# Kernel tuning notes

Measured on AMD Instinct MI355X. Metric: run time of the kernel, lower is better.

The kernel has to match this reference:

```python
import jax, jax.numpy as jnp
from jax import lax
import numpy as np

I_CNN = 2048   # box feature dim
Q_H = 1024     # LSTM hidden
Q_E = 300      # word embedding dim
HID = 512      # gated MLP hidden
B = 256
MAXN = 100
T = 14


def setup_inputs() -> dict:
    key = jax.random.key(0)
    ks = jax.random.split(key, 12)
    w = lambda k, shape: (jax.random.normal(k, shape, dtype=jnp.float32) * 0.02)
    return {
        "wholefeat": jax.random.normal(ks[0], (B, I_CNN), dtype=jnp.float32),
        "pooled": jax.random.normal(ks[1], (B, I_CNN), dtype=jnp.float32),
        "box_feats": jax.random.normal(ks[2], (B, MAXN, I_CNN), dtype=jnp.float32),
        "q_feats": jax.random.normal(ks[3], (B, T, Q_E), dtype=jnp.float32),
        "box_coords": jax.random.uniform(ks[4], (B, MAXN, 4), dtype=jnp.float32),
        "index": jax.random.randint(ks[5], (B,), 1, MAXN + 1),
        # LSTM params (PyTorch layout: gates ordered i,f,g,o)
        "W_ih": w(ks[6], (4 * Q_H, Q_E)),
        "W_hh": w(ks[7], (4 * Q_H, Q_H)),
        "b_ih": jnp.zeros((4 * Q_H,), jnp.float32),
        "b_hh": jnp.zeros((4 * Q_H,), jnp.float32),
        # gated MLP params
        "W_w": w(ks[8], (HID, I_CNN + Q_H)),
        "W_b": jnp.zeros((HID,), jnp.float32),
        "Wp_w": w(ks[9], (HID, I_CNN + Q_H)),
        "Wp_b": jnp.zeros((HID,), jnp.float32),
        "f_w": w(ks[10], (1, HID)),
    }


def _lstm_last(x_tbe, W_ih, W_hh, b_ih, b_hh):
    # x_tbe: [T, B, E] time-major. Returns final hidden state h_T: [B, H].
    H = W_hh.shape[1]
    # precompute input projections for all timesteps: [T, B, 4H]
    xg = jnp.einsum('tbe,ge->tbg', x_tbe, W_ih) + (b_ih + b_hh)

    def step(carry, xt):
        h, c = carry
        gates = xt + h @ W_hh.T                       # [B, 4H]
        i, f, g, o = jnp.split(gates, 4, axis=-1)
        i = jax.nn.sigmoid(i)
        f = jax.nn.sigmoid(f)
        g = jnp.tanh(g)
        o = jax.nn.sigmoid(o)
        c = f * c + i * g
        h = o * jnp.tanh(c)
        return (h, c), None

    h0 = jnp.zeros((x_tbe.shape[1], H), x_tbe.dtype)
    (h, _), _ = lax.scan(step, (h0, h0), xg)
    return h


def reference(wholefeat, pooled, box_feats, q_feats, box_coords, index,
              W_ih, W_hh, b_ih, b_hh, W_w, W_b, Wp_w, Wp_b, f_w):
    # question encoding: last LSTM output per sample -> [B, Q_H]
    q_rnn = _lstm_last(jnp.transpose(q_feats, (1, 0, 2)), W_ih, W_hh, b_ih, b_hh)

    Bn, N, _ = box_feats.shape
    qst = jnp.broadcast_to(q_rnn[:, None, :], (Bn, N, q_rnn.shape[-1]))
    b_full = jnp.concatenate([box_feats, qst], axis=-1)        # [B, N, 3072]

    y_tilde = jnp.tanh(jnp.einsum('bnd,hd->bnh', b_full, W_w) + W_b)
    g = jax.nn.sigmoid(jnp.einsum('bnd,hd->bnh', b_full, Wp_w) + Wp_b)
    si = y_tilde * g                                           # [B, N, HID]
    wsi = jax.nn.sigmoid(jnp.einsum('bnh,oh->bno', si, f_w))[..., 0]  # [B, N]

    # ragged reduction: only the first index[i] boxes of sample i contribute
    mask = (jnp.arange(N)[None, :] < index[:, None]).astype(wsi.dtype)
    return jnp.sum(wsi * mask, axis=1)                         # [B]
```

## Files before the change

### kernel.cpp

```cpp
#include <hip/hip_runtime.h>
#include <cstdint>
#include <cstddef>

#define DEVI __device__ __forceinline__

typedef __attribute__((ext_vector_type(8))) short short8;
typedef __attribute__((ext_vector_type(4))) float f32x4;
typedef __bf16 bf16x8 __attribute__((ext_vector_type(8)));

DEVI float sigf(float x) { return 1.0f / (1.0f + __expf(-x)); }
DEVI float tanh_f(float x) { return 2.0f / (1.0f + __expf(-2.0f * x)) - 1.0f; }

DEVI short f2bf(float x) {
    uint32_t u = __builtin_bit_cast(uint32_t, x);
    u += 0x7FFFu + ((u >> 16) & 1u);
    return (short)(u >> 16);
}
DEVI float bf2f(short s) {
    uint32_t u = ((uint32_t)(unsigned short)s) << 16;
    return __builtin_bit_cast(float, u);
}

DEVI void gload16(const void* g, void* l) {
    __builtin_amdgcn_global_load_lds(
        (const __attribute__((address_space(1))) void*)g,
        (__attribute__((address_space(3))) void*)l, 16, 0, 0);
}

DEVI f32x4 mfma16(short8 a, short8 b, f32x4 c) {
    return __builtin_amdgcn_mfma_f32_16x16x32_bf16(
        __builtin_bit_cast(bf16x8, a), __builtin_bit_cast(bf16x8, b), c, 0, 0, 0);
}


__global__ __launch_bounds__(256) void prep_wstk(const float* __restrict__ Wih,
                                                 const float* __restrict__ Whh,
                                                 const float* __restrict__ bih,
                                                 const float* __restrict__ bhh,
                                                 short* __restrict__ Wstk) {
    int idx = blockIdx.x * 256 + threadIdx.x;
    if (idx >= 4096 * 1344) return;
    int n = idx / 1344, k = idx - n * 1344;
    int hblk = n >> 6, gate = (n >> 4) & 3, hl = n & 15;
    int on = gate * 1024 + hblk * 16 + hl;
    float v = 0.f;
    if (k < 300) v = Wih[on * 300 + k];
    else if (k == 300) v = bih[on] + bhh[on];
    else if (k >= 320) v = Whh[on * 1024 + (k - 320)];
    Wstk[idx] = f2bf(v);
}

__global__ __launch_bounds__(256) void prep_x(const float* __restrict__ q,
                                              short* __restrict__ xb) {
    int idx = blockIdx.x * 256 + threadIdx.x;
    if (idx >= 14 * 256 * 320) return;
    int t = idx / (256 * 320);
    int r = idx - t * 256 * 320;
    int b = r / 320, e = r - b * 320;
    float v = (e < 300) ? q[(b * 14 + t) * 300 + e] : (e == 300 ? 1.0f : 0.0f);
    xb[idx] = f2bf(v);
}

__global__ __launch_bounds__(256) void prep_wcat(const float* __restrict__ Ww,
                                                 const float* __restrict__ Wpw,
                                                 short* __restrict__ Wcat) {
    int idx = blockIdx.x * 256 + threadIdx.x;
    if (idx >= 1024 * 3072) return;
    int n = idx / 3072, k = idx - n * 3072;
    int hg = n >> 5, which = (n >> 4) & 1, hl = n & 15;
    int h = hg * 16 + hl;
    const float* src = which ? Wpw : Ww;
    Wcat[idx] = f2bf(src[h * 3072 + k]);
}

__global__ __launch_bounds__(256) void prep_index(const int* __restrict__ index,
                                                  int* __restrict__ cum,
                                                  int* __restrict__ rowmap,
                                                  int* __restrict__ bmap) {
    __shared__ int s[256];
    int t = threadIdx.x;
    int myidx = index[t];
    s[t] = myidx;
    __syncthreads();
    for (int off = 1; off < 256; off <<= 1) {
        int v = (t >= off) ? s[t - off] : 0;
        __syncthreads();
        s[t] += v;
        __syncthreads();
    }
    cum[t + 1] = s[t];
    if (t == 0) cum[0] = 0;
    int base = s[t] - myidx;
    for (int j = 0; j < myidx; ++j) {
        rowmap[base + j] = t * 100 + j;
        bmap[base + j] = t;
    }
    int Ml = s[255];
    if (t < 128) { rowmap[Ml + t] = 0; bmap[Ml + t] = 0; }
}

__global__ __launch_bounds__(256) void compact_box(const float* __restrict__ box,
                                                   const int* __restrict__ index,
                                                   const int* __restrict__ cum,
                                                   short* __restrict__ Ac) {
    int m = blockIdx.x;
    int b = m / 100, j = m - b * 100;
    if (j >= index[b]) return;
    size_t dr = (size_t)(cum[b] + j);
    int t = threadIdx.x;
    const float* src = box + (size_t)m * 2048 + t * 8;
    float4 v0 = *(const float4*)src;
    float4 v1 = *(const float4*)(src + 4);
    short8 s;
    s[0] = f2bf(v0.x); s[1] = f2bf(v0.y); s[2] = f2bf(v0.z); s[3] = f2bf(v0.w);
    s[4] = f2bf(v1.x); s[5] = f2bf(v1.y); s[6] = f2bf(v1.z); s[7] = f2bf(v1.w);
    *(short8*)&Ac[dr * 2048 + t * 8] = s;
}


__global__ __launch_bounds__(256) void xg_gemm(const short* __restrict__ xb,
                                               const short* __restrict__ Wstk,
                                               short* __restrict__ xg) {
    __shared__ __attribute__((aligned(16))) short As[128 * 64];
    __shared__ __attribute__((aligned(16))) short Bs[128 * 64];
    const int tid = threadIdx.x, l = tid & 63, w = tid >> 6;
    const int n0 = blockIdx.x * 128;
    const int m0 = blockIdx.y * 128;
    const int wm = w >> 1, wn = w & 1;

    const short* asrc[4];
    const short* bsrc[4];
    for (int i = 0; i < 4; i++) {
        int r = w * 32 + i * 8 + (l >> 3);
        int cs = (l & 7) ^ (r & 7);
        asrc[i] = xb + (size_t)(m0 + r) * 320 + cs * 8;
        bsrc[i] = Wstk + (size_t)(n0 + r) * 1344 + cs * 8;
    }

    f32x4 acc[4][4];
    for (int i = 0; i < 4; i++)
        for (int j = 0; j < 4; j++) acc[i][j] = f32x4{0.f, 0.f, 0.f, 0.f};

    for (int kt = 0; kt < 5; ++kt) {
        const int k0 = kt * 64;
        __syncthreads();
        for (int i = 0; i < 4; i++)
            gload16(asrc[i] + k0, &As[(w * 32 + i * 8) * 64]);
        for (int i = 0; i < 4; i++)
            gload16(bsrc[i] + k0, &Bs[(w * 32 + i * 8) * 64]);
        __syncthreads();
        for (int ks = 0; ks < 2; ++ks) {
            short8 a[4], b[4];
            for (int mf = 0; mf < 4; ++mf) {
                int m = wm * 64 + mf * 16 + (l & 15);
                int ca = (ks * 4 + (l >> 4)) ^ (m & 7);
                a[mf] = *(const short8*)&As[m * 64 + ca * 8];
            }
            for (int nf = 0; nf < 4; ++nf) {
                int n = wn * 64 + nf * 16 + (l & 15);
                int cb = (ks * 4 + (l >> 4)) ^ (n & 7);
                b[nf] = *(const short8*)&Bs[n * 64 + cb * 8];
            }
            for (int mf = 0; mf < 4; ++mf)
                for (int nf = 0; nf < 4; ++nf)
                    acc[mf][nf] = mfma16(a[mf], b[nf], acc[mf][nf]);
        }
    }
    const int hl = l & 15, hi = l >> 4;
    for (int mf = 0; mf < 4; ++mf)
        for (int nf = 0; nf < 4; ++nf)
            for (int rg = 0; rg < 4; ++rg) {
                int row = m0 + wm * 64 + mf * 16 + hi * 4 + rg;
                int col = n0 + wn * 64 + nf * 16 + hl;
                xg[(size_t)row * 4096 + col] = f2bf(acc[mf][nf][rg]);
            }
}


__global__ __launch_bounds__(128) void lstm_step(const short* __restrict__ hin,
                                                 const short* __restrict__ Wstk,
                                                 const short* __restrict__ xg_t,
                                                 float* __restrict__ c,
                                                 short* __restrict__ hout,
                                                 int dogemm) {
    __shared__ __attribute__((aligned(16))) short As[2][32 * 128];
    __shared__ __attribute__((aligned(16))) short Bs[2][64 * 128];
    const int tid = threadIdx.x, l = tid & 63, w = tid >> 6;
    const int hi = l >> 4, hl = l & 15;
    const int bid = blockIdx.x;
    const int xcd = bid & 7, ii = bid >> 3;
    const int ny = xcd * 8 + (ii & 7);
    const int mx = ii >> 3;
    const int m0 = mx * 32, n0g = ny * 64;

    f32x4 acc[4];
    for (int i = 0; i < 4; i++) acc[i] = f32x4{0.f, 0.f, 0.f, 0.f};

    if (dogemm) {
        const short* asrc[4];
        const short* bsrc[8];
        for (int i = 0; i < 4; i++) {
            int s = i * 128 + tid;
            int r = s >> 4, cs = s & 15;
            asrc[i] = hin + (size_t)(m0 + r) * 1024 + ((cs ^ (r & 15)) * 8);
        }
        for (int i = 0; i < 8; i++) {
            int s = i * 128 + tid;
            int r = s >> 4, cs = s & 15;
            bsrc[i] = Wstk + (size_t)(n0g + r) * 1344 + 320 + ((cs ^ (r & 15)) * 8);
        }
        for (int i = 0; i < 4; i++) gload16(asrc[i], &As[0][(i * 128 + tid) * 8]);
        for (int i = 0; i < 8; i++) gload16(bsrc[i], &Bs[0][(i * 128 + tid) * 8]);

        for (int kt = 0; kt < 8; ++kt) {
            const int cur = kt & 1;
            if (kt < 7) {
                const int k0 = (kt + 1) * 128;
                for (int i = 0; i < 4; i++)
                    gload16(asrc[i] + k0, &As[cur ^ 1][(i * 128 + tid) * 8]);
                for (int i = 0; i < 8; i++)
                    gload16(bsrc[i] + k0, &Bs[cur ^ 1][(i * 128 + tid) * 8]);
                asm volatile("s_waitcnt vmcnt(12)" ::: "memory");
            } else {
                asm volatile("s_waitcnt vmcnt(0)" ::: "memory");
            }
            __builtin_amdgcn_sched_barrier(0);
            __builtin_amdgcn_s_barrier();
            __builtin_amdgcn_sched_barrier(0);
#pragma unroll
            for (int ks = 0; ks < 4; ++ks) {
                const int mrow = w * 16 + hl;
                const int ca = (ks * 4 + hi) ^ hl;
                short8 a = *(const short8*)&As[cur][mrow * 128 + ca * 8];
#pragma unroll
                for (int nf = 0; nf < 4; ++nf) {
                    const int nrow = nf * 16 + hl;
                    short8 b = *(const short8*)&Bs[cur][nrow * 128 + ca * 8];
                    acc[nf] = mfma16(a, b, acc[nf]);
                }
            }
            __builtin_amdgcn_sched_barrier(0);
            asm volatile("s_waitcnt lgkmcnt(0)" ::: "memory");
            __builtin_amdgcn_s_barrier();
            __builtin_amdgcn_sched_barrier(0);
        }
    }

    const short* xr0 = xg_t + (size_t)(m0 + w * 16 + hi * 4) * 4096 + n0g + hl;
    for (int rg = 0; rg < 4; ++rg) {
        const short* xr = xr0 + (size_t)rg * 4096;
        float ig = acc[0][rg] + bf2f(xr[0]);
        float fg = acc[1][rg] + bf2f(xr[16]);
        float gg = acc[2][rg] + bf2f(xr[32]);
        float og = acc[3][rg] + bf2f(xr[48]);
        size_t off = (size_t)(m0 + w * 16 + hi * 4 + rg) * 1024 + ny * 16 + hl;
        float cn = sigf(fg) * c[off] + sigf(ig) * tanh_f(gg);
        c[off] = cn;
        hout[off] = f2bf(sigf(og) * tanh_f(cn));
    }
}


__global__ __launch_bounds__(256) void mlp_gemm(const short* __restrict__ Ac,
                                                const short* __restrict__ hb,
                                                const short* __restrict__ Wcat,
                                                const int* __restrict__ mliveptr,
                                                const int* __restrict__ bmap,
                                                const float* __restrict__ Wb,
                                                const float* __restrict__ Wpb,
                                                const float* __restrict__ fw,
                                                float* __restrict__ logits) {
    __shared__ __attribute__((aligned(16))) short As[128 * 64];
    __shared__ __attribute__((aligned(16))) short Bs[128 * 64];
    const int Mlive = *mliveptr;
    const int tid = threadIdx.x, l = tid & 63, w = tid >> 6;
    const int bid = blockIdx.x;
    const int xcd = bid & 7, ii = bid >> 3;
    const int x = ii & 7, q = ii >> 3;
    const int y = q * 8 + xcd;
    const int n0 = x * 128, m0 = y * 128;
    if (m0 >= Mlive) return;
    const int wm = w >> 1, wn = w & 1;

    const short* asrc[4];
    const short* hsrc[4];
    const short* bsrc[4];
    for (int i = 0; i < 4; i++) {
        int r = w * 32 + i * 8 + (l >> 3);
        int cs = (l & 7) ^ (r & 7);
        asrc[i] = Ac + (size_t)(m0 + r) * 2048 + cs * 8;
        hsrc[i] = hb + (size_t)bmap[m0 + r] * 1024 + cs * 8;
        bsrc[i] = Wcat + (size_t)(n0 + r) * 3072 + cs * 8;
    }

    f32x4 acc[4][4];
    for (int i = 0; i < 4; i++)
        for (int j = 0; j < 4; j++) acc[i][j] = f32x4{0.f, 0.f, 0.f, 0.f};

    for (int kt = 0; kt < 48; ++kt) {
        const int k0 = kt * 64;
        __syncthreads();
        if (kt < 32) {
            for (int i = 0; i < 4; i++)
                gload16(asrc[i] + k0, &As[(w * 32 + i * 8) * 64]);
        } else {
            const int kq = k0 - 2048;
            for (int i = 0; i < 4; i++)
                gload16(hsrc[i] + kq, &As[(w * 32 + i * 8) * 64]);
        }
        for (int i = 0; i < 4; i++)
            gload16(bsrc[i] + k0, &Bs[(w * 32 + i * 8) * 64]);
        __syncthreads();
        for (int ks = 0; ks < 2; ++ks) {
            short8 a[4], b[4];
            for (int mf = 0; mf < 4; ++mf) {
                int m = wm * 64 + mf * 16 + (l & 15);
                int ca = (ks * 4 + (l >> 4)) ^ (m & 7);
                a[mf] = *(const short8*)&As[m * 64 + ca * 8];
            }
            for (int nf = 0; nf < 4; ++nf) {
                int n = wn * 64 + nf * 16 + (l & 15);
                int cb = (ks * 4 + (l >> 4)) ^ (n & 7);
                b[nf] = *(const short8*)&Bs[n * 64 + cb * 8];
            }
            for (int mf = 0; mf < 4; ++mf)
                for (int nf = 0; nf < 4; ++nf)
                    acc[mf][nf] = mfma16(a[mf], b[nf], acc[mf][nf]);
        }
    }

    const int hl = l & 15, hi = l >> 4;
    for (int mf = 0; mf < 4; ++mf) {
        float part[4] = {0.f, 0.f, 0.f, 0.f};
        for (int p = 0; p < 2; ++p) {
            int ntg = (n0 + wn * 64) / 16 + 2 * p;
            int hg = ntg >> 1;
            int h = hg * 16 + hl;
            float fwv = fw[h], wbv = Wb[h], wpbv = Wpb[h];
            for (int rg = 0; rg < 4; ++rg) {
                float y2 = tanh_f(acc[mf][2 * p][rg] + wbv);
                float g2 = sigf(acc[mf][2 * p + 1][rg] + wpbv);
                part[rg] += y2 * g2 * fwv;
            }
        }
        for (int rg = 0; rg < 4; ++rg) {
            float v = part[rg];
            v += __shfl_xor(v, 1, 64);
            v += __shfl_xor(v, 2, 64);
            v += __shfl_xor(v, 4, 64);
            v += __shfl_xor(v, 8, 64);
            if (hl == 0) {
                int row = m0 + wm * 64 + mf * 16 + hi * 4 + rg;
                atomicAdd(&logits[row], v);
            }
        }
    }
}

__global__ __launch_bounds__(128) void reduce_out(const float* __restrict__ logits,
                                                  const int* __restrict__ index,
                                                  const int* __restrict__ cum,
                                                  float* __restrict__ out) {
    int b = blockIdx.x, t = threadIdx.x;
    int idx = index[b];
    int base = cum[b];
    float v = 0.f;
    if (t < 100 && t < idx) v = sigf(logits[base + t]);
    for (int m = 32; m; m >>= 1) v += __shfl_down(v, m, 64);
    __shared__ float s[2];
    if ((t & 63) == 0) s[t >> 6] = v;
    __syncthreads();
    if (t == 0) out[b] = s[0] + s[1];
}


extern "C" void kernel_launch(void* const* d_in, const int* in_sizes, int n_in,
                              void* d_out, int out_size, void* d_ws, size_t ws_size,
                              hipStream_t stream) {
    (void)in_sizes; (void)n_in; (void)out_size; (void)ws_size;
    const float* box = (const float*)d_in[2];
    const float* qf  = (const float*)d_in[3];
    const int* index = (const int*)d_in[5];
    const float* Wih = (const float*)d_in[6];
    const float* Whh = (const float*)d_in[7];
    const float* bih = (const float*)d_in[8];
    const float* bhh = (const float*)d_in[9];
    const float* Ww  = (const float*)d_in[10];
    const float* Wb  = (const float*)d_in[11];
    const float* Wpw = (const float*)d_in[12];
    const float* Wpb = (const float*)d_in[13];
    const float* fw  = (const float*)d_in[14];

    char* p = (char*)d_ws;
    short* Wstk = (short*)p;  p += (size_t)4096 * 1344 * 2;
    short* Wcat = (short*)p;  p += (size_t)1024 * 3072 * 2;
    short* xb   = (short*)p;  p += (size_t)3584 * 320 * 2;
    short* hb0  = (short*)p;  p += (size_t)256 * 1024 * 2;
    short* hb1  = (short*)p;  p += (size_t)256 * 1024 * 2;
    short* xg   = (short*)p;  p += (size_t)3584 * 4096 * 2;
    float* c    = (float*)p;  p += (size_t)256 * 1024 * 4;
    int*   cum  = (int*)p;    p += 260 * 4;
    int*   rowmap = (int*)p;  p += (size_t)(25600 + 128) * 4;
    int*   bmap = (int*)p;    p += (size_t)(25600 + 128) * 4;
    float* lgt  = (float*)p;  p += (size_t)25600 * 4;
    p = (char*)(((uintptr_t)p + 255) & ~(uintptr_t)255);
    short* Ac   = (short*)p;  p += (size_t)25600 * 2048 * 2;

    hipMemsetAsync(hb0, 0, (size_t)256 * 1024 * 2, stream);
    hipMemsetAsync(c, 0, (size_t)256 * 1024 * 4, stream);
    hipMemsetAsync(lgt, 0, (size_t)25600 * 4, stream);

    prep_index<<<1, 256, 0, stream>>>(index, cum, rowmap, bmap);
    prep_wstk<<<(4096 * 1344) / 256, 256, 0, stream>>>(Wih, Whh, bih, bhh, Wstk);
    prep_x<<<(14 * 256 * 320) / 256, 256, 0, stream>>>(qf, xb);
    prep_wcat<<<(1024 * 3072) / 256, 256, 0, stream>>>(Ww, Wpw, Wcat);

    compact_box<<<25600, 256, 0, stream>>>(box, index, cum, Ac);

    xg_gemm<<<dim3(32, 28), 256, 0, stream>>>(xb, Wstk, xg);

    short* hbuf[2] = {hb0, hb1};
    for (int t = 0; t < 14; ++t) {
        lstm_step<<<512, 128, 0, stream>>>(
            hbuf[t & 1], Wstk, xg + (size_t)t * 256 * 4096, c,
            hbuf[(t & 1) ^ 1], t == 0 ? 0 : 1);
    }

    mlp_gemm<<<1600, 256, 0, stream>>>(Ac, hb0, Wcat, cum + 256, bmap,
                                       Wb, Wpb, fw, lgt);
    reduce_out<<<256, 128, 0, stream>>>(lgt, index, cum, (float*)d_out);
}
```

Measured before the change: 351.7 us.

## Fuse prep kernels and memsets, double-buffer MLP GEMM LDS loads

Merges the three weight/input conversion kernels and three memsets into a single vectorized prep_all kernel, which cuts launch count and uses 8-wide stores. It also drops the unused rowmap output from prep_index. mlp_gemm now double-buffers its shared-memory tiles, issuing the next k-tile's global_load_lds before computing the current one and waiting with explicit vmcnt, so loads overlap MFMA work. LDS use doubles to 64KB per block, which may lower occupancy.

New measurement: 341.1 us. -3.0%, faster.

```diff
diff --git a/kernel.cpp b/kernel.cpp
--- a/kernel.cpp
+++ b/kernel.cpp
@@ -33,49 +33,85 @@
 }
 
 
-__global__ __launch_bounds__(256) void prep_wstk(const float* __restrict__ Wih,
-                                                 const float* __restrict__ Whh,
-                                                 const float* __restrict__ bih,
-                                                 const float* __restrict__ bhh,
-                                                 short* __restrict__ Wstk) {
-    int idx = blockIdx.x * 256 + threadIdx.x;
-    if (idx >= 4096 * 1344) return;
-    int n = idx / 1344, k = idx - n * 1344;
-    int hblk = n >> 6, gate = (n >> 4) & 3, hl = n & 15;
-    int on = gate * 1024 + hblk * 16 + hl;
-    float v = 0.f;
-    if (k < 300) v = Wih[on * 300 + k];
-    else if (k == 300) v = bih[on] + bhh[on];
-    else if (k >= 320) v = Whh[on * 1024 + (k - 320)];
-    Wstk[idx] = f2bf(v);
-}
-
-__global__ __launch_bounds__(256) void prep_x(const float* __restrict__ q,
-                                              short* __restrict__ xb) {
-    int idx = blockIdx.x * 256 + threadIdx.x;
-    if (idx >= 14 * 256 * 320) return;
-    int t = idx / (256 * 320);
-    int r = idx - t * 256 * 320;
-    int b = r / 320, e = r - b * 320;
-    float v = (e < 300) ? q[(b * 14 + t) * 300 + e] : (e == 300 ? 1.0f : 0.0f);
-    xb[idx] = f2bf(v);
-}
-
-__global__ __launch_bounds__(256) void prep_wcat(const float* __restrict__ Ww,
-                                                 const float* __restrict__ Wpw,
-                                                 short* __restrict__ Wcat) {
-    int idx = blockIdx.x * 256 + threadIdx.x;
-    if (idx >= 1024 * 3072) return;
-    int n = idx / 3072, k = idx - n * 3072;
-    int hg = n >> 5, which = (n >> 4) & 1, hl = n & 15;
-    int h = hg * 16 + hl;
-    const float* src = which ? Wpw : Ww;
-    Wcat[idx] = f2bf(src[h * 3072 + k]);
+#define W_SLOTS   688128
+#define WC_SLOTS  393216
+#define XB_SLOTS  143360
+#define HB_SLOTS  32768
+#define C_SLOTS   65536
+#define LG_SLOTS  6400
+#define PREP_TOT  (W_SLOTS + WC_SLOTS + XB_SLOTS + HB_SLOTS + C_SLOTS + LG_SLOTS)
+
+__global__ __launch_bounds__(256) void prep_all(const float* __restrict__ Wih,
+                                                const float* __restrict__ Whh,
+                                                const float* __restrict__ bih,
+                                                const float* __restrict__ bhh,
+                                                const float* __restrict__ Ww,
+                                                const float* __restrict__ Wpw,
+                                                const float* __restrict__ q,
+                                                short* __restrict__ Wstk,
+                                                short* __restrict__ Wcat,
+                                                short* __restrict__ xb,
+                                                short* __restrict__ hb0,
+                                                float* __restrict__ c,
+                                                float* __restrict__ lgt) {
+    int s = blockIdx.x * 256 + threadIdx.x;
+    if (s < W_SLOTS) {
+        int n = s / 168, c8 = s - n * 168, kb = c8 * 8;
+        int hblk = n >> 6, gate = (n >> 4) & 3, hl = n & 15;
+        int on = gate * 1024 + hblk * 16 + hl;
+        short8 o;
+#pragma unroll
+        for (int e = 0; e < 8; ++e) {
+            int k = kb + e;
+            float v;
+            if (k < 300) v = Wih[on * 300 + k];
+            else if (k == 300) v = bih[on] + bhh[on];
+            else if (k < 320) v = 0.f;
+            else v = Whh[on * 1024 + (k - 320)];
+            o[e] = f2bf(v);
+        }
+        *(short8*)&Wstk[n * 1344 + kb] = o;
+        return;
+    }
+    s -= W_SLOTS;
+    if (s < WC_SLOTS) {
+        int n = s / 384, c8 = s - n * 384, kb = c8 * 8;
+        int hg = n >> 5, which = (n >> 4) & 1, hl = n & 15;
+        int h = hg * 16 + hl;
+        const float* src = (which ? Wpw : Ww) + (size_t)h * 3072 + kb;
+        float4 v0 = *(const float4*)src;
+        float4 v1 = *(const float4*)(src + 4);
+        short8 o;
+        o[0] = f2bf(v0.x); o[1] = f2bf(v0.y); o[2] = f2bf(v0.z); o[3] = f2bf(v0.w);
+        o[4] = f2bf(v1.x); o[5] = f2bf(v1.y); o[6] = f2bf(v1.z); o[7] = f2bf(v1.w);
+        *(short8*)&Wcat[(size_t)n * 3072 + kb] = o;
+        return;
+    }
+    s -= WC_SLOTS;
+    if (s < XB_SLOTS) {
+        int row = s / 40, c8 = s - row * 40, eb = c8 * 8;
+        int t = row / 256, b = row - t * 256;
+        const float* qr = q + (size_t)(b * 14 + t) * 300;
+        short8 o;
+#pragma unroll
+        for (int e = 0; e < 8; ++e) {
+            int ee = eb + e;
+            float v = (ee < 300) ? qr[ee] : (ee == 300 ? 1.0f : 0.0f);
+            o[e] = f2bf(v);
+        }
+        *(short8*)&xb[(size_t)row * 320 + eb] = o;
+        return;
+    }
+    s -= XB_SLOTS;
+    if (s < HB_SLOTS) { ((short8*)hb0)[s] = short8{0,0,0,0,0,0,0,0}; return; }
+    s -= HB_SLOTS;
+    if (s < C_SLOTS) { ((f32x4*)c)[s] = f32x4{0.f,0.f,0.f,0.f}; return; }
+    s -= C_SLOTS;
+    if (s < LG_SLOTS) { ((f32x4*)lgt)[s] = f32x4{0.f,0.f,0.f,0.f}; return; }
 }
 
 __global__ __launch_bounds__(256) void prep_index(const int* __restrict__ index,
                                                   int* __restrict__ cum,
-                                                  int* __restrict__ rowmap,
                                                   int* __restrict__ bmap) {
     __shared__ int s[256];
     int t = threadIdx.x;
@@ -91,12 +127,9 @@
     cum[t + 1] = s[t];
     if (t == 0) cum[0] = 0;
     int base = s[t] - myidx;
-    for (int j = 0; j < myidx; ++j) {
-        rowmap[base + j] = t * 100 + j;
-        bmap[base + j] = t;
-    }
+    for (int j = 0; j < myidx; ++j) bmap[base + j] = t;
     int Ml = s[255];
-    if (t < 128) { rowmap[Ml + t] = 0; bmap[Ml + t] = 0; }
+    if (t < 128) bmap[Ml + t] = 0;
 }
 
 __global__ __launch_bounds__(256) void compact_box(const float* __restrict__ box,
@@ -270,8 +303,8 @@
                                                 const float* __restrict__ Wpb,
                                                 const float* __restrict__ fw,
                                                 float* __restrict__ logits) {
-    __shared__ __attribute__((aligned(16))) short As[128 * 64];
-    __shared__ __attribute__((aligned(16))) short Bs[128 * 64];
+    __shared__ __attribute__((aligned(16))) short As[2][128 * 64];
+    __shared__ __attribute__((aligned(16))) short Bs[2][128 * 64];
     const int Mlive = *mliveptr;
     const int tid = threadIdx.x, l = tid & 63, w = tid >> 6;
     const int bid = blockIdx.x;
@@ -285,48 +318,64 @@
     const short* asrc[4];
     const short* hsrc[4];
     const short* bsrc[4];
+    int ldso[4];
     for (int i = 0; i < 4; i++) {
         int r = w * 32 + i * 8 + (l >> 3);
         int cs = (l & 7) ^ (r & 7);
         asrc[i] = Ac + (size_t)(m0 + r) * 2048 + cs * 8;
         hsrc[i] = hb + (size_t)bmap[m0 + r] * 1024 + cs * 8;
         bsrc[i] = Wcat + (size_t)(n0 + r) * 3072 + cs * 8;
+        ldso[i] = (w * 32 + i * 8) * 64;
     }
 
     f32x4 acc[4][4];
     for (int i = 0; i < 4; i++)
         for (int j = 0; j < 4; j++) acc[i][j] = f32x4{0.f, 0.f, 0.f, 0.f};
 
+    for (int i = 0; i < 4; i++) gload16(asrc[i], &As[0][ldso[i]]);
+    for (int i = 0; i < 4; i++) gload16(bsrc[i], &Bs[0][ldso[i]]);
+
     for (int kt = 0; kt < 48; ++kt) {
-        const int k0 = kt * 64;
-        __syncthreads();
-        if (kt < 32) {
+        const int cur = kt & 1;
+        if (kt < 47) {
+            const int k1 = (kt + 1) * 64;
+            if (kt + 1 < 32) {
+                for (int i = 0; i < 4; i++)
+                    gload16(asrc[i] + k1, &As[cur ^ 1][ldso[i]]);
+            } else {
+                const int kq = k1 - 2048;
+                for (int i = 0; i < 4; i++)
+                    gload16(hsrc[i] + kq, &As[cur ^ 1][ldso[i]]);
+            }
             for (int i = 0; i < 4; i++)
-                gload16(asrc[i] + k0, &As[(w * 32 + i * 8) * 64]);
+                gload16(bsrc[i] + k1, &Bs[cur ^ 1][ldso[i]]);
+            asm volatile("s_waitcnt vmcnt(8)" ::: "memory");
         } else {
-            const int kq = k0 - 2048;
-            for (int i = 0; i < 4; i++)
-                gload16(hsrc[i] + kq, &As[(w * 32 + i * 8) * 64]);
-        }
-        for (int i = 0; i < 4; i++)
-            gload16(bsrc[i] + k0, &Bs[(w * 32 + i * 8) * 64]);
-        __syncthreads();
+            asm volatile("s_waitcnt vmcnt(0)" ::: "memory");
+        }
+        __builtin_amdgcn_sched_barrier(0);
+        __builtin_amdgcn_s_barrier();
+        __builtin_amdgcn_sched_barrier(0);
         for (int ks = 0; ks < 2; ++ks) {
             short8 a[4], b[4];
             for (int mf = 0; mf < 4; ++mf) {
                 int m = wm * 64 + mf * 16 + (l & 15);
                 int ca = (ks * 4 + (l >> 4)) ^ (m & 7);
-                a[mf] = *(const short8*)&As[m * 64 + ca * 8];
+                a[mf] = *(const short8*)&As[cur][m * 64 + ca * 8];
             }
             for (int nf = 0; nf < 4; ++nf) {
                 int n = wn * 64 + nf * 16 + (l & 15);
                 int cb = (ks * 4 + (l >> 4)) ^ (n & 7);
-                b[nf] = *(const short8*)&Bs[n * 64 + cb * 8];
+                b[nf] = *(const short8*)&Bs[cur][n * 64 + cb * 8];
             }
             for (int mf = 0; mf < 4; ++mf)
                 for (int nf = 0; nf < 4; ++nf)
                     acc[mf][nf] = mfma16(a[mf], b[nf], acc[mf][nf]);
         }
+        __builtin_amdgcn_sched_barrier(0);
+        asm volatile("s_waitcnt lgkmcnt(0)" ::: "memory");
+        __builtin_amdgcn_s_barrier();
+        __builtin_amdgcn_sched_barrier(0);
     }
 
     const int hl = l & 15, hi = l >> 4;
@@ -400,20 +449,14 @@
     short* xg   = (short*)p;  p += (size_t)3584 * 4096 * 2;
     float* c    = (float*)p;  p += (size_t)256 * 1024 * 4;
     int*   cum  = (int*)p;    p += 260 * 4;
-    int*   rowmap = (int*)p;  p += (size_t)(25600 + 128) * 4;
     int*   bmap = (int*)p;    p += (size_t)(25600 + 128) * 4;
     float* lgt  = (float*)p;  p += (size_t)25600 * 4;
     p = (char*)(((uintptr_t)p + 255) & ~(uintptr_t)255);
     short* Ac   = (short*)p;  p += (size_t)25600 * 2048 * 2;
 
-    hipMemsetAsync(hb0, 0, (size_t)256 * 1024 * 2, stream);
-    hipMemsetAsync(c, 0, (size_t)256 * 1024 * 4, stream);
-    hipMemsetAsync(lgt, 0, (size_t)25600 * 4, stream);
-
-    prep_index<<<1, 256, 0, stream>>>(index, cum, rowmap, bmap);
-    prep_wstk<<<(4096 * 1344) / 256, 256, 0, stream>>>(Wih, Whh, bih, bhh, Wstk);
-    prep_x<<<(14 * 256 * 320) / 256, 256, 0, stream>>>(qf, xb);
-    prep_wcat<<<(1024 * 3072) / 256, 256, 0, stream>>>(Ww, Wpw, Wcat);
+    prep_index<<<1, 256, 0, stream>>>(index, cum, bmap);
+    prep_all<<<(PREP_TOT + 255) / 256, 256, 0, stream>>>(
+        Wih, Whh, bih, bhh, Ww, Wpw, qf, Wstk, Wcat, xb, hb0, c, lgt);
 
     compact_box<<<25600, 256, 0, stream>>>(box, index, cum, Ac);
 
```
